# Kernel optimization log

Hardware: AMD Instinct MI355X
Metric: run time of the kernel (lower is better)

## Reference

```python
import jax, jax.numpy as jnp
import numpy as np

B = 256        # graphs in batch
N_PER = 512    # nodes per graph (uniform)
D = 256        # in_dim
DEG = 16       # avg degree
RATIO = 0.5


def setup_inputs() -> dict:
    key = jax.random.key(0)
    k1, k2, k3, k4 = jax.random.split(key, 4)
    N = B * N_PER
    e_per = N_PER * DEG
    x = jax.random.normal(k1, (N, D), dtype=jnp.float32)
    # edges confined within each graph (DGL batched-graph structure)
    src = jax.random.randint(k2, (B, e_per), 0, N_PER)
    dst = jax.random.randint(k3, (B, e_per), 0, N_PER)
    offs = jnp.arange(B, dtype=jnp.int32)[:, None] * N_PER
    src = (src + offs).reshape(-1).astype(jnp.int32)
    dst = (dst + offs).reshape(-1).astype(jnp.int32)
    W = jax.random.normal(k4, (D, 1), dtype=jnp.float32) / np.sqrt(D)
    b = jnp.zeros((1,), dtype=jnp.float32)
    num_nodes = jnp.full((B,), N_PER, dtype=jnp.int32)
    return {"x": x, "W": W, "b": b, "src": src, "dst": dst, "num_nodes": num_nodes}


def reference(x, W, b, src, dst, num_nodes):
    N, d = x.shape
    bsz = num_nodes.shape[0]
    n = N // bsz                     # uniform nodes per graph -> static
    k = int(np.ceil(RATIO * n))      # nodes kept per graph (static)

    # ---- GraphConv(in_dim, 1), DGL default norm='both':
    # score = D_in^{-1/2} A D_out^{-1/2} (x W) + b   (W applied first: out_dim < in_dim)
    ones_e = jnp.ones(src.shape, dtype=x.dtype)
    deg_out = jax.ops.segment_sum(ones_e, src, num_segments=N)
    deg_in = jax.ops.segment_sum(ones_e, dst, num_segments=N)
    h = x @ W                                              # [N, 1]
    h = h * jax.lax.rsqrt(jnp.clip(deg_out, 1.0))[:, None]
    agg = jax.ops.segment_sum(h[src], dst, num_segments=N) # [N, 1]
    score = (agg * jax.lax.rsqrt(jnp.clip(deg_in, 1.0))[:, None] + b)[:, 0]  # [N]

    # ---- topk per graph: dense [B, n] buffer is just a reshape (uniform graphs),
    # sort descending + take first k  ==  lax.top_k
    dense = score.reshape(bsz, n)
    _, idx = jax.lax.top_k(dense, k)                       # [B, k] descending
    perm = (idx + jnp.arange(bsz)[:, None] * n).reshape(-1)  # global node ids [B*k]

    # ---- gather + scale: feature[perm] * tanh(score[perm])
    feat = x[perm] * jnp.tanh(score[perm])[:, None]        # [B*k, D]

    # ---- node_subgraph: edges whose both endpoints survive
    keep = jnp.zeros((N,), dtype=bool).at[perm].set(True)
    edge_mask = keep[src] & keep[dst]                      # [E]
    next_num_nodes = jnp.full((bsz,), k, dtype=jnp.int32)
    return feat, perm, edge_mask, next_num_nodes
```

## Files before the change

kernel.cpp:

```cpp
#include <hip/hip_runtime.h>
#include <math.h>

#define BB    256
#define NPER  512
#define DD    256
#define KK    256
#define EPG   (NPER * 16)
#define NN    (BB * NPER)
#define EE    (BB * EPG)

typedef float vf4 __attribute__((ext_vector_type(4)));

__global__ __launch_bounds__(1024) void k_fused(
        const float* __restrict__ x,
        const float* __restrict__ W,
        const float* __restrict__ b,
        const int* __restrict__ src, const int* __restrict__ dst,
        float* __restrict__ feat, float* __restrict__ out_perm,
        float* __restrict__ emask, float* __restrict__ nnn) {
    __shared__ unsigned int es2[EPG / 2];
    __shared__ unsigned int ed2[EPG / 2];
    __shared__ int   degs[NPER];
    __shared__ int   degd[NPER];
    __shared__ float hl[NPER];
    __shared__ float aggl[NPER];
    __shared__ float scl[NPER];
    __shared__ unsigned long long keys[NPER];
    __shared__ float keepf[NPER];
    __shared__ int   sel[KK];
    __shared__ float tsv[KK];

    const int g = blockIdx.x;
    const int t = threadIdx.x;
    const int wave = t >> 6;
    const int lane = t & 63;
    const int nbase = g << 9;

    const int4* s4 = (const int4*)(src + (size_t)g * EPG);
    const int4* d4 = (const int4*)(dst + (size_t)g * EPG);
    int4 sva = s4[t], dva = d4[t];
    int4 svb = s4[t + 1024], dvb = d4[t + 1024];

    if (t < NPER) { degs[t] = 0; degd[t] = 0; aggl[t] = 0.0f; keepf[t] = 0.0f; }

    {
        const float4 wv = ((const float4*)W)[lane];
        const float4* xb = (const float4*)(x + ((size_t)(nbase + (wave << 5)) << 8));
        #pragma unroll
        for (int it = 0; it < 8; ++it) {
            const float4* p = xb + (it << 8);
            float4 a0 = p[lane];
            float4 a1 = p[64 + lane];
            float4 a2 = p[128 + lane];
            float4 a3 = p[192 + lane];
            float d0 = a0.x * wv.x + a0.y * wv.y + a0.z * wv.z + a0.w * wv.w;
            float d1 = a1.x * wv.x + a1.y * wv.y + a1.z * wv.z + a1.w * wv.w;
            float d2 = a2.x * wv.x + a2.y * wv.y + a2.z * wv.z + a2.w * wv.w;
            float d3 = a3.x * wv.x + a3.y * wv.y + a3.z * wv.z + a3.w * wv.w;
            #pragma unroll
            for (int off = 32; off > 0; off >>= 1) {
                d0 += __shfl_down(d0, off, 64);
                d1 += __shfl_down(d1, off, 64);
                d2 += __shfl_down(d2, off, 64);
                d3 += __shfl_down(d3, off, 64);
            }
            if (lane == 0) {
                const int r = (wave << 5) + (it << 2);
                hl[r]     = d0;
                hl[r + 1] = d1;
                hl[r + 2] = d2;
                hl[r + 3] = d3;
            }
        }
    }
    __syncthreads();

    {
        unsigned int a0 = (unsigned int)(sva.x - nbase), a1 = (unsigned int)(sva.y - nbase);
        unsigned int a2 = (unsigned int)(sva.z - nbase), a3 = (unsigned int)(sva.w - nbase);
        es2[t * 2]     = a0 | (a1 << 16);
        es2[t * 2 + 1] = a2 | (a3 << 16);
        atomicAdd(&degs[a0], 1); atomicAdd(&degs[a1], 1);
        atomicAdd(&degs[a2], 1); atomicAdd(&degs[a3], 1);
        unsigned int c0 = (unsigned int)(dva.x - nbase), c1 = (unsigned int)(dva.y - nbase);
        unsigned int c2 = (unsigned int)(dva.z - nbase), c3 = (unsigned int)(dva.w - nbase);
        ed2[t * 2]     = c0 | (c1 << 16);
        ed2[t * 2 + 1] = c2 | (c3 << 16);
        atomicAdd(&degd[c0], 1); atomicAdd(&degd[c1], 1);
        atomicAdd(&degd[c2], 1); atomicAdd(&degd[c3], 1);
    }
    {
        int i = t + 1024;
        unsigned int a0 = (unsigned int)(svb.x - nbase), a1 = (unsigned int)(svb.y - nbase);
        unsigned int a2 = (unsigned int)(svb.z - nbase), a3 = (unsigned int)(svb.w - nbase);
        es2[i * 2]     = a0 | (a1 << 16);
        es2[i * 2 + 1] = a2 | (a3 << 16);
        atomicAdd(&degs[a0], 1); atomicAdd(&degs[a1], 1);
        atomicAdd(&degs[a2], 1); atomicAdd(&degs[a3], 1);
        unsigned int c0 = (unsigned int)(dvb.x - nbase), c1 = (unsigned int)(dvb.y - nbase);
        unsigned int c2 = (unsigned int)(dvb.z - nbase), c3 = (unsigned int)(dvb.w - nbase);
        ed2[i * 2]     = c0 | (c1 << 16);
        ed2[i * 2 + 1] = c2 | (c3 << 16);
        atomicAdd(&degd[c0], 1); atomicAdd(&degd[c1], 1);
        atomicAdd(&degd[c2], 1); atomicAdd(&degd[c3], 1);
    }
    __syncthreads();

    if (t < NPER) hl[t] = hl[t] * rsqrtf(fmaxf((float)degs[t], 1.0f));
    __syncthreads();

    #pragma unroll
    for (int i = t; i < EPG / 2; i += 1024) {
        unsigned int sp = es2[i], dp = ed2[i];
        atomicAdd(&aggl[dp & 0xFFFFu], hl[sp & 0xFFFFu]);
        atomicAdd(&aggl[dp >> 16],     hl[sp >> 16]);
    }
    __syncthreads();

    unsigned long long key = 0;
    if (t < NPER) {
        float sc = aggl[t] * rsqrtf(fmaxf((float)degd[t], 1.0f)) + b[0];
        scl[t] = sc;
        unsigned int u = __float_as_uint(sc);
        u = (u & 0x80000000u) ? ~u : (u | 0x80000000u);
        key = ((unsigned long long)u << 32) |
              (unsigned long long)(0xFFFFFFFFu - (unsigned)t);
    }
    __syncthreads();

    for (int kk = 2; kk <= NPER; kk <<= 1) {
        for (int j = kk >> 1; j > 0; j >>= 1) {
            if (j >= 64) {
                __syncthreads();
                if (t < NPER) keys[t] = key;
                __syncthreads();
                if (t < NPER) {
                    unsigned long long c = keys[t ^ j];
                    bool lower = ((t & j) == 0);
                    bool up    = ((t & kk) == 0);
                    bool takeMax = (up == lower);
                    key = takeMax ? (key >= c ? key : c)
                                  : (key >= c ? c : key);
                }
            } else {
                if (t < NPER) {
                    unsigned long long c = __shfl_xor(key, j, 64);
                    bool lower = ((t & j) == 0);
                    bool up    = ((t & kk) == 0);
                    bool takeMax = (up == lower);
                    key = takeMax ? (key >= c ? key : c)
                                  : (key >= c ? c : key);
                }
            }
        }
    }

    if (t < KK) {
        int idx = (int)(0xFFFFFFFFu - (unsigned int)(key & 0xFFFFFFFFull));
        out_perm[(g << 8) + t] = (float)(nbase + idx);
        sel[t] = idx;
        tsv[t] = tanhf(scl[idx]);
        keepf[idx] = 1.0f;
    }
    __syncthreads();

    #pragma unroll
    for (int it = 0; it < 16; it += 2) {
        const int j0 = wave * 16 + it, j1 = j0 + 1;
        const int l0 = sel[j0], l1 = sel[j1];
        const float s0 = tsv[j0], s1 = tsv[j1];
        const float4* q0 = (const float4*)(x + ((size_t)(nbase + l0) << 8));
        const float4* q1 = (const float4*)(x + ((size_t)(nbase + l1) << 8));
        float4 v0 = q0[lane], v1 = q1[lane];
        vf4 o0 = { v0.x * s0, v0.y * s0, v0.z * s0, v0.w * s0 };
        vf4 o1 = { v1.x * s1, v1.y * s1, v1.z * s1, v1.w * s1 };
        vf4* f0 = (vf4*)(feat + ((size_t)((g << 8) + j0) << 8)) + lane;
        vf4* f1 = (vf4*)(feat + ((size_t)((g << 8) + j1) << 8)) + lane;
        __builtin_nontemporal_store(o0, f0);
        __builtin_nontemporal_store(o1, f1);
    }

    vf4* em4 = (vf4*)(emask + ((size_t)g << 13));
    #pragma unroll
    for (int i = t; i < EPG / 4; i += 1024) {
        unsigned int sp0 = es2[i * 2], sp1 = es2[i * 2 + 1];
        unsigned int dp0 = ed2[i * 2], dp1 = ed2[i * 2 + 1];
        vf4 m;
        m.x = keepf[sp0 & 0xFFFFu] * keepf[dp0 & 0xFFFFu];
        m.y = keepf[sp0 >> 16]     * keepf[dp0 >> 16];
        m.z = keepf[sp1 & 0xFFFFu] * keepf[dp1 & 0xFFFFu];
        m.w = keepf[sp1 >> 16]     * keepf[dp1 >> 16];
        __builtin_nontemporal_store(m, &em4[i]);
    }
    if (g == 0 && t < BB) nnn[t] = (float)KK;
}

extern "C" void kernel_launch(void* const* d_in, const int* in_sizes, int n_in,
                              void* d_out, int out_size, void* d_ws, size_t ws_size,
                              hipStream_t stream) {
    const float* x   = (const float*)d_in[0];
    const float* W   = (const float*)d_in[1];
    const float* b   = (const float*)d_in[2];
    const int*   src = (const int*)d_in[3];
    const int*   dst = (const int*)d_in[4];

    float* out   = (float*)d_out;
    float* feat  = out;
    float* operm = feat + (size_t)BB * KK * DD;
    float* emask = operm + (size_t)BB * KK;
    float* nnn   = emask + (size_t)EE;

    k_fused<<<BB, 1024, 0, stream>>>(x, W, b, src, dst,
                                     feat, operm, emask, nnn);
}
```

Baseline: 254.6 us.

## Warp-specialize waves: half compute xW, half parse edges; batch gather loads

Waves 0-7 now compute the x·W projection for all 512 nodes while waves 8-15 concurrently load the edge lists, pack them into LDS and build the degree histograms, where previously every wave did both phases one after the other. The edge-mask write is moved onto the upper waves before the feature gather, and the gather now issues 8 row loads per wave before the scaled stores to raise memory-level parallelism. A redundant barrier before the sort is removed and launch_bounds gains a min-blocks hint. In exchange, the x-projection runs on half the waves with a longer per-wave loop, and it adds an extra barrier after the LDS init.

```diff
diff --git a/kernel.cpp b/kernel.cpp
--- a/kernel.cpp
+++ b/kernel.cpp
@@ -11,7 +11,7 @@
 
 typedef float vf4 __attribute__((ext_vector_type(4)));
 
-__global__ __launch_bounds__(1024) void k_fused(
+__global__ __launch_bounds__(1024, 4) void k_fused(
         const float* __restrict__ x,
         const float* __restrict__ W,
         const float* __restrict__ b,
@@ -36,18 +36,17 @@
     const int lane = t & 63;
     const int nbase = g << 9;
 
-    const int4* s4 = (const int4*)(src + (size_t)g * EPG);
-    const int4* d4 = (const int4*)(dst + (size_t)g * EPG);
-    int4 sva = s4[t], dva = d4[t];
-    int4 svb = s4[t + 1024], dvb = d4[t + 1024];
-
-    if (t < NPER) { degs[t] = 0; degd[t] = 0; aggl[t] = 0.0f; keepf[t] = 0.0f; }
-
-    {
+    if (t >= 512) {
+        const int tt = t - 512;
+        degs[tt] = 0; degd[tt] = 0; aggl[tt] = 0.0f; keepf[tt] = 0.0f;
+    }
+    __syncthreads();
+
+    if (wave < 8) {
         const float4 wv = ((const float4*)W)[lane];
-        const float4* xb = (const float4*)(x + ((size_t)(nbase + (wave << 5)) << 8));
-        #pragma unroll
-        for (int it = 0; it < 8; ++it) {
+        const float4* xb = (const float4*)(x + ((size_t)(nbase + (wave << 6)) << 8));
+        #pragma unroll 4
+        for (int it = 0; it < 16; ++it) {
             const float4* p = xb + (it << 8);
             float4 a0 = p[lane];
             float4 a1 = p[64 + lane];
@@ -65,44 +64,34 @@
                 d3 += __shfl_down(d3, off, 64);
             }
             if (lane == 0) {
-                const int r = (wave << 5) + (it << 2);
+                const int r = (wave << 6) + (it << 2);
                 hl[r]     = d0;
                 hl[r + 1] = d1;
                 hl[r + 2] = d2;
                 hl[r + 3] = d3;
             }
         }
-    }
-    __syncthreads();
-
-    {
-        unsigned int a0 = (unsigned int)(sva.x - nbase), a1 = (unsigned int)(sva.y - nbase);
-        unsigned int a2 = (unsigned int)(sva.z - nbase), a3 = (unsigned int)(sva.w - nbase);
-        es2[t * 2]     = a0 | (a1 << 16);
-        es2[t * 2 + 1] = a2 | (a3 << 16);
-        atomicAdd(&degs[a0], 1); atomicAdd(&degs[a1], 1);
-        atomicAdd(&degs[a2], 1); atomicAdd(&degs[a3], 1);
-        unsigned int c0 = (unsigned int)(dva.x - nbase), c1 = (unsigned int)(dva.y - nbase);
-        unsigned int c2 = (unsigned int)(dva.z - nbase), c3 = (unsigned int)(dva.w - nbase);
-        ed2[t * 2]     = c0 | (c1 << 16);
-        ed2[t * 2 + 1] = c2 | (c3 << 16);
-        atomicAdd(&degd[c0], 1); atomicAdd(&degd[c1], 1);
-        atomicAdd(&degd[c2], 1); atomicAdd(&degd[c3], 1);
-    }
-    {
-        int i = t + 1024;
-        unsigned int a0 = (unsigned int)(svb.x - nbase), a1 = (unsigned int)(svb.y - nbase);
-        unsigned int a2 = (unsigned int)(svb.z - nbase), a3 = (unsigned int)(svb.w - nbase);
-        es2[i * 2]     = a0 | (a1 << 16);
-        es2[i * 2 + 1] = a2 | (a3 << 16);
-        atomicAdd(&degs[a0], 1); atomicAdd(&degs[a1], 1);
-        atomicAdd(&degs[a2], 1); atomicAdd(&degs[a3], 1);
-        unsigned int c0 = (unsigned int)(dvb.x - nbase), c1 = (unsigned int)(dvb.y - nbase);
-        unsigned int c2 = (unsigned int)(dvb.z - nbase), c3 = (unsigned int)(dvb.w - nbase);
-        ed2[i * 2]     = c0 | (c1 << 16);
-        ed2[i * 2 + 1] = c2 | (c3 << 16);
-        atomicAdd(&degd[c0], 1); atomicAdd(&degd[c1], 1);
-        atomicAdd(&degd[c2], 1); atomicAdd(&degd[c3], 1);
+    } else {
+        const int tt = t - 512;
+        const int4* s4 = (const int4*)(src + (size_t)g * EPG);
+        const int4* d4 = (const int4*)(dst + (size_t)g * EPG);
+        #pragma unroll
+        for (int c = 0; c < 4; ++c) {
+            const int i = tt + (c << 9);
+            int4 sv = s4[i], dv = d4[i];
+            unsigned int a0 = (unsigned int)(sv.x - nbase), a1 = (unsigned int)(sv.y - nbase);
+            unsigned int a2 = (unsigned int)(sv.z - nbase), a3 = (unsigned int)(sv.w - nbase);
+            es2[i * 2]     = a0 | (a1 << 16);
+            es2[i * 2 + 1] = a2 | (a3 << 16);
+            atomicAdd(&degs[a0], 1); atomicAdd(&degs[a1], 1);
+            atomicAdd(&degs[a2], 1); atomicAdd(&degs[a3], 1);
+            unsigned int c0 = (unsigned int)(dv.x - nbase), c1 = (unsigned int)(dv.y - nbase);
+            unsigned int c2 = (unsigned int)(dv.z - nbase), c3 = (unsigned int)(dv.w - nbase);
+            ed2[i * 2]     = c0 | (c1 << 16);
+            ed2[i * 2 + 1] = c2 | (c3 << 16);
+            atomicAdd(&degd[c0], 1); atomicAdd(&degd[c1], 1);
+            atomicAdd(&degd[c2], 1); atomicAdd(&degd[c3], 1);
+        }
     }
     __syncthreads();
 
@@ -126,7 +115,6 @@
         key = ((unsigned long long)u << 32) |
               (unsigned long long)(0xFFFFFFFFu - (unsigned)t);
     }
-    __syncthreads();
 
     for (int kk = 2; kk <= NPER; kk <<= 1) {
         for (int j = kk >> 1; j > 0; j >>= 1) {
@@ -164,33 +152,42 @@
     }
     __syncthreads();
 
-    #pragma unroll
-    for (int it = 0; it < 16; it += 2) {
-        const int j0 = wave * 16 + it, j1 = j0 + 1;
-        const int l0 = sel[j0], l1 = sel[j1];
-        const float s0 = tsv[j0], s1 = tsv[j1];
-        const float4* q0 = (const float4*)(x + ((size_t)(nbase + l0) << 8));
-        const float4* q1 = (const float4*)(x + ((size_t)(nbase + l1) << 8));
-        float4 v0 = q0[lane], v1 = q1[lane];
-        vf4 o0 = { v0.x * s0, v0.y * s0, v0.z * s0, v0.w * s0 };
-        vf4 o1 = { v1.x * s1, v1.y * s1, v1.z * s1, v1.w * s1 };
-        vf4* f0 = (vf4*)(feat + ((size_t)((g << 8) + j0) << 8)) + lane;
-        vf4* f1 = (vf4*)(feat + ((size_t)((g << 8) + j1) << 8)) + lane;
-        __builtin_nontemporal_store(o0, f0);
-        __builtin_nontemporal_store(o1, f1);
-    }
-
-    vf4* em4 = (vf4*)(emask + ((size_t)g << 13));
-    #pragma unroll
-    for (int i = t; i < EPG / 4; i += 1024) {
-        unsigned int sp0 = es2[i * 2], sp1 = es2[i * 2 + 1];
-        unsigned int dp0 = ed2[i * 2], dp1 = ed2[i * 2 + 1];
-        vf4 m;
-        m.x = keepf[sp0 & 0xFFFFu] * keepf[dp0 & 0xFFFFu];
-        m.y = keepf[sp0 >> 16]     * keepf[dp0 >> 16];
-        m.z = keepf[sp1 & 0xFFFFu] * keepf[dp1 & 0xFFFFu];
-        m.w = keepf[sp1 >> 16]     * keepf[dp1 >> 16];
-        __builtin_nontemporal_store(m, &em4[i]);
+    if (wave >= 8) {
+        const int tt = t - 512;
+        vf4* em4 = (vf4*)(emask + ((size_t)g << 13));
+        #pragma unroll
+        for (int c = 0; c < 4; ++c) {
+            const int i = tt + (c << 9);
+            unsigned int sp0 = es2[i * 2], sp1 = es2[i * 2 + 1];
+            unsigned int dp0 = ed2[i * 2], dp1 = ed2[i * 2 + 1];
+            vf4 m;
+            m.x = keepf[sp0 & 0xFFFFu] * keepf[dp0 & 0xFFFFu];
+            m.y = keepf[sp0 >> 16]     * keepf[dp0 >> 16];
+            m.z = keepf[sp1 & 0xFFFFu] * keepf[dp1 & 0xFFFFu];
+            m.w = keepf[sp1 >> 16]     * keepf[dp1 >> 16];
+            __builtin_nontemporal_store(m, &em4[i]);
+        }
+    }
+
+    {
+        const int base = wave << 4;
+        #pragma unroll
+        for (int ch = 0; ch < 2; ++ch) {
+            const int j0 = base + (ch << 3);
+            int   l[8]; float s[8]; float4 v[8];
+            #pragma unroll
+            for (int u = 0; u < 8; ++u) { l[u] = sel[j0 + u]; s[u] = tsv[j0 + u]; }
+            #pragma unroll
+            for (int u = 0; u < 8; ++u) {
+                v[u] = ((const float4*)(x + ((size_t)(nbase + l[u]) << 8)))[lane];
+            }
+            #pragma unroll
+            for (int u = 0; u < 8; ++u) {
+                vf4 o = { v[u].x * s[u], v[u].y * s[u], v[u].z * s[u], v[u].w * s[u] };
+                __builtin_nontemporal_store(
+                    o, (vf4*)(feat + ((size_t)((g << 8) + j0 + u) << 8)) + lane);
+            }
+        }
     }
     if (g == 0 && t < BB) nnn[t] = (float)KK;
 }
```

After: 254.6 us. No clear change (-0.0%).
